# Performance work log

Measured on AMD Instinct MI355X. Metric: run time of the kernel, lower is better.

The kernel has to match this reference:

```python
import jax, jax.numpy as jnp
import numpy as np

B, T, D, H = 4, 2048, 512, 8
DK = D // H


def setup_inputs() -> dict:
    key0 = jax.random.key(0)
    ks = jax.random.split(key0, 16)
    s = 1.0 / np.sqrt(D)
    inp = {
        "query": jax.random.normal(ks[0], (B, T, D), jnp.float32),
        "key": jax.random.normal(ks[1], (B, T, D), jnp.float32),
        "value": jax.random.normal(ks[2], (B, T, D), jnp.float32),
        "mask": jnp.ones((B, 1, T), jnp.int32),
        "pos_emb": jax.random.normal(ks[3], (1, T, D), jnp.float32),
        "Wq": jax.random.normal(ks[4], (D, D), jnp.float32) * s,
        "bq": jnp.zeros((D,), jnp.float32),
        "Wk": jax.random.normal(ks[5], (D, D), jnp.float32) * s,
        "bk": jnp.zeros((D,), jnp.float32),
        "Wv": jax.random.normal(ks[6], (D, D), jnp.float32) * s,
        "bv": jnp.zeros((D,), jnp.float32),
        "Wo": jax.random.normal(ks[7], (D, D), jnp.float32) * s,
        "bo": jnp.zeros((D,), jnp.float32),
        "Wp": jax.random.normal(ks[8], (D, D), jnp.float32) * s,  # linear_pos, no bias
        "pos_bias_u": jax.random.normal(ks[9], (H, DK), jnp.float32) * 0.05,
        "pos_bias_v": jax.random.normal(ks[10], (H, DK), jnp.float32) * 0.05,
    }
    return inp


def reference(query, key, value, mask, pos_emb, Wq, bq, Wk, bk, Wv, bv, Wo, bo, Wp, pos_bias_u, pos_bias_v):
    b, t1, d = query.shape
    h, dk = pos_bias_u.shape
    # projections -> (b, t, h, dk)
    q = (query @ Wq.T + bq).reshape(b, t1, h, dk)
    k = (key @ Wk.T + bk).reshape(b, -1, h, dk)
    v = (value @ Wv.T + bv).reshape(b, -1, h, dk)
    # positional projection (n_batch_pos == 1): (t2, h, dk)
    p = (pos_emb @ Wp.T).reshape(pos_emb.shape[0], -1, h, dk)[0]
    # content score (a+c) and position score (b+d); NOTE: this repo's forward
    # does not apply rel_shift -- matrix_bd is used directly.
    matrix_ac = jnp.einsum("bthd,bshd->bhts", q + pos_bias_u, k)
    matrix_bd = jnp.einsum("bthd,shd->bhts", q + pos_bias_v, p)
    scores = (matrix_ac + matrix_bd) / np.sqrt(dk)
    # mask: (b, 1, t2) -> (b, 1, 1, t2); masked where mask == 0
    m = (mask[:, None, :, :] == 0)
    scores = jnp.where(m, -jnp.inf, scores)
    attn = jax.nn.softmax(scores, axis=-1)
    attn = jnp.where(m, 0.0, attn)
    x = jnp.einsum("bhts,bshd->bthd", attn, v).reshape(b, t1, h * dk)
    return x @ Wo.T + bo
```

## Files before the change

### kernel.cpp

```cpp
#include <hip/hip_runtime.h>

typedef __bf16 bf16;
typedef __attribute__((ext_vector_type(8))) __bf16 bf16x8;
typedef __attribute__((ext_vector_type(4))) __bf16 bf16x4;
typedef __attribute__((ext_vector_type(4))) float f32x4;

#define NB 4
#define NT 2048
#define ND 512
#define NH 8
#define NDK 64
#define GAMMA 0.1803368801111204f

#define OFF_XQ 0ull
#define OFF_XK 4194304ull
#define OFF_XV 8388608ull
#define OFF_XP 12582912ull
#define OFF_WQ 13631488ull
#define OFF_WK 13893632ull
#define OFF_WV 14155776ull
#define OFF_WP 14417920ull
#define OFF_WO 14680064ull
#define OFF_QU 14942208ull
#define OFF_QV 19136512ull
#define OFF_KB 23330816ull
#define OFF_VT 27525120ull
#define OFF_PB 31719424ull
#define OFF_OA OFF_XQ

__global__ __launch_bounds__(256) void convert_bf16(
    const float* __restrict__ q, const float* __restrict__ k,
    const float* __restrict__ v, const float* __restrict__ p,
    const float* __restrict__ wq, const float* __restrict__ wk,
    const float* __restrict__ wv, const float* __restrict__ wp,
    const float* __restrict__ wo, bf16* __restrict__ dst) {
  int bid = blockIdx.x;
  const float* src;
  size_t doff;
  if (bid < 2048) { src = q; doff = OFF_XQ; }
  else if (bid < 4096) { src = k; doff = OFF_XK; bid -= 2048; }
  else if (bid < 6144) { src = v; doff = OFF_XV; bid -= 4096; }
  else if (bid < 6656) { src = p; doff = OFF_XP; bid -= 6144; }
  else if (bid < 6784) { src = wq; doff = OFF_WQ; bid -= 6656; }
  else if (bid < 6912) { src = wk; doff = OFF_WK; bid -= 6784; }
  else if (bid < 7040) { src = wv; doff = OFF_WV; bid -= 6912; }
  else if (bid < 7168) { src = wp; doff = OFF_WP; bid -= 7040; }
  else { src = wo; doff = OFF_WO; bid -= 7168; }
  size_t base = (size_t)bid * 2048 + threadIdx.x * 8;
  float4 x0 = *(const float4*)(src + base);
  float4 x1 = *(const float4*)(src + base + 4);
  bf16x8 o;
  o[0] = (bf16)x0.x; o[1] = (bf16)x0.y; o[2] = (bf16)x0.z; o[3] = (bf16)x0.w;
  o[4] = (bf16)x1.x; o[5] = (bf16)x1.y; o[6] = (bf16)x1.z; o[7] = (bf16)x1.w;
  *(bf16x8*)(dst + doff + base) = o;
}

__device__ __forceinline__ void flush_tile(const bf16* LT, bf16* dst, int bm,
                                           int bn, int tid, bool isP) {
#pragma unroll
  for (int i = 0; i < 8; i++) {
    int chunk = tid + i * 256;
    int mm = chunk >> 4, c8 = (chunk & 15) * 8;
    bf16x8 vv = *(const bf16x8*)&LT[mm * 144 + c8];
    int n = bn + c8, h = n >> 6, d = n & 63;
    int gm = bm + mm;
    size_t gidx;
    if (isP)
      gidx = ((size_t)h * NT + gm) * NDK + d;
    else
      gidx = ((size_t)((gm >> 11) * NH + h) * NT + (gm & 2047)) * NDK + d;
    *(bf16x8*)(dst + gidx) = vv;
  }
}

__global__ __launch_bounds__(256) void proj_fused(
    const bf16* __restrict__ Xq, const bf16* __restrict__ Xk,
    const bf16* __restrict__ Xv, const bf16* __restrict__ Xp,
    const bf16* __restrict__ wq, const bf16* __restrict__ wk,
    const bf16* __restrict__ wv, const bf16* __restrict__ wp,
    const float* __restrict__ bq, const float* __restrict__ bk,
    const float* __restrict__ bv, const float* __restrict__ pu,
    const float* __restrict__ pv, bf16* __restrict__ Qu, bf16* __restrict__ Qv,
    bf16* __restrict__ Kb, bf16* __restrict__ Vt, bf16* __restrict__ Pb) {
  __shared__ bf16 smem[2][128][72];

  const int bid = blockIdx.x;
  const int mode = (bid >= 768) ? 3 : (bid >> 8);
  const int idx = (mode == 3) ? bid - 768 : (bid & 255);
  const int bm = (idx >> 2) * 128, bn = (idx & 3) * 128;

  const bf16* X;
  const bf16* W;
  if (mode == 0) { X = Xq; W = wq; }
  else if (mode == 1) { X = Xk; W = wk; }
  else if (mode == 2) { X = Xv; W = wv; }
  else { X = Xp; W = wp; }

  const int tid = threadIdx.x;
  const int l = tid & 63, w = tid >> 6;
  const int q = l >> 4, ln = l & 15;
  const int wm = (w >> 1) * 64, wn = (w & 1) * 64;

  f32x4 acc[4][4];
#pragma unroll
  for (int i = 0; i < 4; i++)
#pragma unroll
    for (int j = 0; j < 4; j++) acc[i][j] = (f32x4){0.f, 0.f, 0.f, 0.f};

  const int srow = tid >> 3, scol = (tid & 7) * 8;
  const size_t abase = (size_t)(bm + srow) * 512 + scol;
  const size_t bbase = (size_t)(bn + srow) * 512 + scol;

  bf16x8 ar[4], br[4];
#pragma unroll
  for (int i = 0; i < 4; i++) {
    ar[i] = *(const bf16x8*)(X + abase + (size_t)i * 32 * 512);
    br[i] = *(const bf16x8*)(W + bbase + (size_t)i * 32 * 512);
  }

  for (int k0 = 0; k0 < 512; k0 += 64) {
    __syncthreads();
#pragma unroll
    for (int i = 0; i < 4; i++) {
      *(bf16x8*)&smem[0][srow + i * 32][scol] = ar[i];
      *(bf16x8*)&smem[1][srow + i * 32][scol] = br[i];
    }
    if (k0 + 64 < 512) {
#pragma unroll
      for (int i = 0; i < 4; i++) {
        ar[i] = *(const bf16x8*)(X + abase + k0 + 64 + (size_t)i * 32 * 512);
        br[i] = *(const bf16x8*)(W + bbase + k0 + 64 + (size_t)i * 32 * 512);
      }
    }
    __syncthreads();
#pragma unroll
    for (int kc = 0; kc < 2; kc++) {
      bf16x8 af[4], bfr[4];
#pragma unroll
      for (int rt = 0; rt < 4; rt++)
        af[rt] = *(const bf16x8*)&smem[0][wm + rt * 16 + ln][kc * 32 + q * 8];
#pragma unroll
      for (int ct = 0; ct < 4; ct++)
        bfr[ct] = *(const bf16x8*)&smem[1][wn + ct * 16 + ln][kc * 32 + q * 8];
#pragma unroll
      for (int rt = 0; rt < 4; rt++)
#pragma unroll
        for (int ct = 0; ct < 4; ct++)
          acc[rt][ct] = __builtin_amdgcn_mfma_f32_16x16x32_bf16(
              af[rt], bfr[ct], acc[rt][ct], 0, 0, 0);
    }
  }

  bf16* LT = &smem[0][0][0];

  if (mode == 2) {
    __syncthreads();
#pragma unroll
    for (int ct = 0; ct < 4; ct++) {
      const int n = bn + wn + ct * 16 + ln;
      const float bvn = bv[n];
#pragma unroll
      for (int rt = 0; rt < 4; rt++) {
        bf16x4 t4;
#pragma unroll
        for (int r = 0; r < 4; r++) t4[r] = (bf16)(acc[rt][ct][r] + bvn);
        *(bf16x4*)&LT[(wn + ct * 16 + ln) * 144 + wm + rt * 16 + q * 4] = t4;
      }
    }
    __syncthreads();
    const int b = bm >> 11, tb = bm & 2047;
#pragma unroll
    for (int i = 0; i < 8; i++) {
      int chunk = tid + i * 256;
      int nn = chunk >> 4, m8 = (chunk & 15) * 8;
      int n = bn + nn, h = n >> 6, d = n & 63;
      size_t gidx = (((size_t)(b * NH + h)) * NDK + d) * NT + tb + m8;
      *(bf16x8*)(Vt + gidx) = *(const bf16x8*)&LT[nn * 144 + m8];
    }
    return;
  }

  if (mode == 0) {
    float addu[4], addv[4];
#pragma unroll
    for (int ct = 0; ct < 4; ct++) {
      int n = bn + wn + ct * 16 + ln;
      float bb = bq[n];
      addu[ct] = bb + pu[n];
      addv[ct] = bb + pv[n];
    }
    __syncthreads();
#pragma unroll
    for (int rt = 0; rt < 4; rt++)
#pragma unroll
      for (int ct = 0; ct < 4; ct++)
#pragma unroll
        for (int r = 0; r < 4; r++)
          LT[(wm + rt * 16 + q * 4 + r) * 144 + wn + ct * 16 + ln] =
              (bf16)((acc[rt][ct][r] + addu[ct]) * GAMMA);
    __syncthreads();
    flush_tile(LT, Qu, bm, bn, tid, false);
    __syncthreads();
#pragma unroll
    for (int rt = 0; rt < 4; rt++)
#pragma unroll
      for (int ct = 0; ct < 4; ct++)
#pragma unroll
        for (int r = 0; r < 4; r++)
          LT[(wm + rt * 16 + q * 4 + r) * 144 + wn + ct * 16 + ln] =
              (bf16)((acc[rt][ct][r] + addv[ct]) * GAMMA);
    __syncthreads();
    flush_tile(LT, Qv, bm, bn, tid, false);
    return;
  }

  {
    float bb[4];
#pragma unroll
    for (int ct = 0; ct < 4; ct++) {
      int n = bn + wn + ct * 16 + ln;
      bb[ct] = (mode == 1) ? bk[n] : 0.f;
    }
    __syncthreads();
#pragma unroll
    for (int rt = 0; rt < 4; rt++)
#pragma unroll
      for (int ct = 0; ct < 4; ct++)
#pragma unroll
        for (int r = 0; r < 4; r++)
          LT[(wm + rt * 16 + q * 4 + r) * 144 + wn + ct * 16 + ln] =
              (bf16)(acc[rt][ct][r] + bb[ct]);
    __syncthreads();
    flush_tile(LT, (mode == 1) ? Kb : Pb, bm, bn, tid, mode == 3);
  }
}

__global__ __launch_bounds__(256) void flash(
    const bf16* __restrict__ Qu, const bf16* __restrict__ Qv,
    const bf16* __restrict__ Kb, const bf16* __restrict__ Pb,
    const bf16* __restrict__ Vt, const int* __restrict__ mask,
    bf16* __restrict__ Oa) {
  __shared__ bf16 sK[64][136];
  __shared__ bf16 sVt[64][72];
  __shared__ bf16 sPT[4][16][40];
  __shared__ float sbias[64];

  const int tid = threadIdx.x;
  const int l = tid & 63, w = tid >> 6;
  const int q = l >> 4, ln = l & 15;
  const int t0 = blockIdx.x * 64;
  const int bh = blockIdx.y;
  const int b = bh >> 3;

  const size_t qrow = (((size_t)bh) * NT + t0 + w * 16 + ln) * NDK;
  bf16x8 qf[4];
  qf[0] = *(const bf16x8*)(Qu + qrow + q * 8);
  qf[1] = *(const bf16x8*)(Qu + qrow + 32 + q * 8);
  qf[2] = *(const bf16x8*)(Qv + qrow + q * 8);
  qf[3] = *(const bf16x8*)(Qv + qrow + 32 + q * 8);

  int okacc = 1;
  for (int i = tid; i < NT; i += 256) okacc &= (mask[b * NT + i] != 0);
  const int allones = __syncthreads_and(okacc);

  float lsum = 0.f;
  f32x4 O[4];
#pragma unroll
  for (int dt = 0; dt < 4; dt++) O[dt] = (f32x4){0.f, 0.f, 0.f, 0.f};

  const bf16* Krow = Kb + ((size_t)bh) * NT * NDK;
  const bf16* Prow = Pb + ((size_t)(bh & 7)) * NT * NDK;
  const bf16* Vrow = Vt + ((size_t)bh) * NDK * NT;

  const int krow = tid >> 4, kcc = tid & 15;
  const int vrow = tid >> 3, vcol = (tid & 7) * 8;
  const bf16* kpsrc = (kcc < 8) ? (Krow + kcc * 8) : (Prow + (kcc - 8) * 8);

  bf16x8 rk[4], rv[2];
#pragma unroll
  for (int i = 0; i < 4; i++)
    rk[i] = *(const bf16x8*)(kpsrc + (size_t)(krow + i * 16) * NDK);
#pragma unroll
  for (int i = 0; i < 2; i++)
    rv[i] = *(const bf16x8*)(Vrow + (size_t)(vrow + i * 32) * NT + vcol);

  for (int s0 = 0; s0 < NT; s0 += 64) {
    __syncthreads();
#pragma unroll
    for (int i = 0; i < 4; i++) *(bf16x8*)&sK[krow + i * 16][kcc * 8] = rk[i];
#pragma unroll
    for (int i = 0; i < 2; i++) *(bf16x8*)&sVt[vrow + i * 32][vcol] = rv[i];
    if (s0 + 64 < NT) {
#pragma unroll
      for (int i = 0; i < 4; i++)
        rk[i] =
            *(const bf16x8*)(kpsrc + (size_t)(s0 + 64 + krow + i * 16) * NDK);
#pragma unroll
      for (int i = 0; i < 2; i++)
        rv[i] = *(const bf16x8*)(Vrow + (size_t)(vrow + i * 32) * NT + s0 + 64 +
                                 vcol);
    }
    if (!allones && tid < 64)
      sbias[tid] = mask[b * NT + s0 + tid] ? 0.f : -1e30f;
    __syncthreads();

    f32x4 ST[4];
#pragma unroll
    for (int ct = 0; ct < 4; ct++) {
      ST[ct] = (f32x4){0.f, 0.f, 0.f, 0.f};
#pragma unroll
      for (int kc = 0; kc < 4; kc++) {
        bf16x8 kf = *(const bf16x8*)&sK[ct * 16 + ln][kc * 32 + q * 8];
        ST[ct] = __builtin_amdgcn_mfma_f32_16x16x32_bf16(kf, qf[kc], ST[ct], 0,
                                                         0, 0);
      }
    }
    if (!allones) {
#pragma unroll
      for (int ct = 0; ct < 4; ct++) {
        float4 bb = *(const float4*)&sbias[ct * 16 + q * 4];
        ST[ct][0] += bb.x;
        ST[ct][1] += bb.y;
        ST[ct][2] += bb.z;
        ST[ct][3] += bb.w;
      }
    }
#pragma unroll
    for (int c = 0; c < 2; c++) {
#pragma unroll
      for (int cc = 0; cc < 2; cc++) {
        const int ct = c * 2 + cc;
        unsigned u0 = __builtin_bit_cast(unsigned,
                                         __builtin_amdgcn_exp2f(ST[ct][0]));
        unsigned u1 = __builtin_bit_cast(unsigned,
                                         __builtin_amdgcn_exp2f(ST[ct][1]));
        unsigned u2 = __builtin_bit_cast(unsigned,
                                         __builtin_amdgcn_exp2f(ST[ct][2]));
        unsigned u3 = __builtin_bit_cast(unsigned,
                                         __builtin_amdgcn_exp2f(ST[ct][3]));
        lsum += __builtin_bit_cast(float, u0 & 0xffff0000u) +
                __builtin_bit_cast(float, u1 & 0xffff0000u) +
                __builtin_bit_cast(float, u2 & 0xffff0000u) +
                __builtin_bit_cast(float, u3 & 0xffff0000u);
        uint2 pk;
        pk.x = (u0 >> 16) | (u1 & 0xffff0000u);
        pk.y = (u2 >> 16) | (u3 & 0xffff0000u);
        *(uint2*)&sPT[w][ln][cc * 16 + q * 4] = pk;
      }
      bf16x8 paf = *(const bf16x8*)&sPT[w][ln][q * 8];
#pragma unroll
      for (int dt = 0; dt < 4; dt++) {
        bf16x8 vb = *(const bf16x8*)&sVt[dt * 16 + ln][c * 32 + q * 8];
        O[dt] =
            __builtin_amdgcn_mfma_f32_16x16x32_bf16(paf, vb, O[dt], 0, 0, 0);
      }
    }
  }

  float s = lsum;
  s += __shfl_xor(s, 16);
  s += __shfl_xor(s, 32);
#pragma unroll
  for (int r = 0; r < 4; r++) {
    float dr = __shfl(s, q * 4 + r);
    float inv = (dr > 0.f) ? 1.f / dr : 0.f;
    int t = t0 + w * 16 + q * 4 + r;
    size_t base = (((size_t)b * NT + t) * NH + (bh & 7)) * NDK;
#pragma unroll
    for (int dt = 0; dt < 4; dt++)
      Oa[base + dt * 16 + ln] = (bf16)(O[dt][r] * inv);
  }
}

__global__ __launch_bounds__(256) void out_gemm(const bf16* __restrict__ A,
                                                const bf16* __restrict__ W,
                                                const float* __restrict__ bias,
                                                float* __restrict__ out) {
  __shared__ bf16 sA[128][72];
  __shared__ bf16 sB[64][72];

  const int tid = threadIdx.x;
  const int l = tid & 63, w = tid >> 6;
  const int q = l >> 4, ln = l & 15;
  const int wm = (w >> 1) * 64, wn = (w & 1) * 32;
  const int bm = blockIdx.x * 128, bn = blockIdx.y * 64;

  f32x4 acc[4][2];
#pragma unroll
  for (int i = 0; i < 4; i++)
#pragma unroll
    for (int j = 0; j < 2; j++) acc[i][j] = (f32x4){0.f, 0.f, 0.f, 0.f};

  const int srow = tid >> 3, scol = (tid & 7) * 8;
  const size_t abase = (size_t)(bm + srow) * 512 + scol;
  const size_t bbase = (size_t)(bn + srow) * 512 + scol;

  bf16x8 ar[4], br[2];
#pragma unroll
  for (int i = 0; i < 4; i++)
    ar[i] = *(const bf16x8*)(A + abase + (size_t)i * 32 * 512);
#pragma unroll
  for (int i = 0; i < 2; i++)
    br[i] = *(const bf16x8*)(W + bbase + (size_t)i * 32 * 512);

  for (int k0 = 0; k0 < 512; k0 += 64) {
    __syncthreads();
#pragma unroll
    for (int i = 0; i < 4; i++) *(bf16x8*)&sA[srow + i * 32][scol] = ar[i];
#pragma unroll
    for (int i = 0; i < 2; i++) *(bf16x8*)&sB[srow + i * 32][scol] = br[i];
    if (k0 + 64 < 512) {
#pragma unroll
      for (int i = 0; i < 4; i++)
        ar[i] = *(const bf16x8*)(A + abase + k0 + 64 + (size_t)i * 32 * 512);
#pragma unroll
      for (int i = 0; i < 2; i++)
        br[i] = *(const bf16x8*)(W + bbase + k0 + 64 + (size_t)i * 32 * 512);
    }
    __syncthreads();
#pragma unroll
    for (int kc = 0; kc < 2; kc++) {
      bf16x8 af[4], bfr[2];
#pragma unroll
      for (int rt = 0; rt < 4; rt++)
        af[rt] = *(const bf16x8*)&sA[wm + rt * 16 + ln][kc * 32 + q * 8];
#pragma unroll
      for (int ct = 0; ct < 2; ct++)
        bfr[ct] = *(const bf16x8*)&sB[wn + ct * 16 + ln][kc * 32 + q * 8];
#pragma unroll
      for (int rt = 0; rt < 4; rt++)
#pragma unroll
        for (int ct = 0; ct < 2; ct++)
          acc[rt][ct] = __builtin_amdgcn_mfma_f32_16x16x32_bf16(
              af[rt], bfr[ct], acc[rt][ct], 0, 0, 0);
    }
  }

#pragma unroll
  for (int rt = 0; rt < 4; rt++)
#pragma unroll
    for (int ct = 0; ct < 2; ct++) {
      const int n = bn + wn + ct * 16 + ln;
      const float bias_n = bias[n];
#pragma unroll
      for (int r = 0; r < 4; r++) {
        const int m = bm + wm + rt * 16 + q * 4 + r;
        out[(size_t)m * 512 + n] = acc[rt][ct][r] + bias_n;
      }
    }
}

extern "C" void kernel_launch(void* const* d_in, const int* in_sizes, int n_in,
                              void* d_out, int out_size, void* d_ws,
                              size_t ws_size, hipStream_t stream) {
  const float* query = (const float*)d_in[0];
  const float* key = (const float*)d_in[1];
  const float* value = (const float*)d_in[2];
  const int* mask = (const int*)d_in[3];
  const float* pos = (const float*)d_in[4];
  const float* Wq = (const float*)d_in[5];
  const float* bq = (const float*)d_in[6];
  const float* Wk = (const float*)d_in[7];
  const float* bk = (const float*)d_in[8];
  const float* Wv = (const float*)d_in[9];
  const float* bv = (const float*)d_in[10];
  const float* Wo = (const float*)d_in[11];
  const float* bo = (const float*)d_in[12];
  const float* Wp = (const float*)d_in[13];
  const float* pu = (const float*)d_in[14];
  const float* pv = (const float*)d_in[15];
  float* out = (float*)d_out;

  bf16* ws = (bf16*)d_ws;
  dim3 blk(256);
  convert_bf16<<<dim3(7296), blk, 0, stream>>>(query, key, value, pos, Wq, Wk,
                                               Wv, Wp, Wo, ws);
  proj_fused<<<dim3(832), blk, 0, stream>>>(
      ws + OFF_XQ, ws + OFF_XK, ws + OFF_XV, ws + OFF_XP, ws + OFF_WQ,
      ws + OFF_WK, ws + OFF_WV, ws + OFF_WP, bq, bk, bv, pu, pv, ws + OFF_QU,
      ws + OFF_QV, ws + OFF_KB, ws + OFF_VT, ws + OFF_PB);
  flash<<<dim3(32, 32), blk, 0, stream>>>(ws + OFF_QU, ws + OFF_QV,
                                          ws + OFF_KB, ws + OFF_PB,
                                          ws + OFF_VT, mask, ws + OFF_OA);
  out_gemm<<<dim3(64, 8), blk, 0, stream>>>(ws + OFF_OA, ws + OFF_WO, bo, out);
}
```

Baseline: 248.0 us.

## Enlarge flash blocks to 1024 threads and vectorize projection epilogue stores

The flash kernel now runs 16 waves per block covering 256 query rows, so each K/P/V tile staged in shared memory is reused by four times as many query rows, and each thread loads one K row chunk and at most one V chunk per step. The projection GEMM swaps the MFMA operands for non-V modes so each lane holds four consecutive columns. That lets the epilogue write bf16x4 vectors with float4 bias loads, and the padded LDS strides change to reduce bank conflicts. In exchange, the large flash blocks lower per-block scheduling flexibility, give only 256 blocks, and put register pressure under 1024-thread launch bounds.

```diff
diff --git a/kernel.cpp b/kernel.cpp
--- a/kernel.cpp
+++ b/kernel.cpp
@@ -11,6 +11,7 @@
 #define NH 8
 #define NDK 64
 #define GAMMA 0.1803368801111204f
+#define LTS 152
 
 #define OFF_XQ 0ull
 #define OFF_XK 4194304ull
@@ -61,7 +62,7 @@
   for (int i = 0; i < 8; i++) {
     int chunk = tid + i * 256;
     int mm = chunk >> 4, c8 = (chunk & 15) * 8;
-    bf16x8 vv = *(const bf16x8*)&LT[mm * 144 + c8];
+    bf16x8 vv = *(const bf16x8*)&LT[mm * LTS + c8];
     int n = bn + c8, h = n >> 6, d = n & 63;
     int gm = bm + mm;
     size_t gidx;
@@ -82,7 +83,7 @@
     const float* __restrict__ bv, const float* __restrict__ pu,
     const float* __restrict__ pv, bf16* __restrict__ Qu, bf16* __restrict__ Qv,
     bf16* __restrict__ Kb, bf16* __restrict__ Vt, bf16* __restrict__ Pb) {
-  __shared__ bf16 smem[2][128][72];
+  __shared__ bf16 smem[2][128][76];
 
   const int bid = blockIdx.x;
   const int mode = (bid >= 768) ? 3 : (bid >> 8);
@@ -142,12 +143,21 @@
 #pragma unroll
       for (int ct = 0; ct < 4; ct++)
         bfr[ct] = *(const bf16x8*)&smem[1][wn + ct * 16 + ln][kc * 32 + q * 8];
-#pragma unroll
-      for (int rt = 0; rt < 4; rt++)
-#pragma unroll
-        for (int ct = 0; ct < 4; ct++)
-          acc[rt][ct] = __builtin_amdgcn_mfma_f32_16x16x32_bf16(
-              af[rt], bfr[ct], acc[rt][ct], 0, 0, 0);
+      if (mode == 2) {
+#pragma unroll
+        for (int rt = 0; rt < 4; rt++)
+#pragma unroll
+          for (int ct = 0; ct < 4; ct++)
+            acc[rt][ct] = __builtin_amdgcn_mfma_f32_16x16x32_bf16(
+                af[rt], bfr[ct], acc[rt][ct], 0, 0, 0);
+      } else {
+#pragma unroll
+        for (int rt = 0; rt < 4; rt++)
+#pragma unroll
+          for (int ct = 0; ct < 4; ct++)
+            acc[rt][ct] = __builtin_amdgcn_mfma_f32_16x16x32_bf16(
+                bfr[ct], af[rt], acc[rt][ct], 0, 0, 0);
+      }
     }
   }
 
@@ -164,7 +174,7 @@
         bf16x4 t4;
 #pragma unroll
         for (int r = 0; r < 4; r++) t4[r] = (bf16)(acc[rt][ct][r] + bvn);
-        *(bf16x4*)&LT[(wn + ct * 16 + ln) * 144 + wm + rt * 16 + q * 4] = t4;
+        *(bf16x4*)&LT[(wn + ct * 16 + ln) * LTS + wm + rt * 16 + q * 4] = t4;
       }
     }
     __syncthreads();
@@ -175,84 +185,98 @@
       int nn = chunk >> 4, m8 = (chunk & 15) * 8;
       int n = bn + nn, h = n >> 6, d = n & 63;
       size_t gidx = (((size_t)(b * NH + h)) * NDK + d) * NT + tb + m8;
-      *(bf16x8*)(Vt + gidx) = *(const bf16x8*)&LT[nn * 144 + m8];
+      *(bf16x8*)(Vt + gidx) = *(const bf16x8*)&LT[nn * LTS + m8];
     }
     return;
   }
 
+  const int mloc = wm + ln;
+  const int nloc = wn + q * 4;
+
   if (mode == 0) {
-    float addu[4], addv[4];
+    float4 addu4[4], addv4[4];
 #pragma unroll
     for (int ct = 0; ct < 4; ct++) {
-      int n = bn + wn + ct * 16 + ln;
-      float bb = bq[n];
-      addu[ct] = bb + pu[n];
-      addv[ct] = bb + pv[n];
+      int n0 = bn + nloc + ct * 16;
+      float4 bb = *(const float4*)(bq + n0);
+      float4 uu = *(const float4*)(pu + n0);
+      float4 vv = *(const float4*)(pv + n0);
+      addu4[ct] = make_float4(bb.x + uu.x, bb.y + uu.y, bb.z + uu.z, bb.w + uu.w);
+      addv4[ct] = make_float4(bb.x + vv.x, bb.y + vv.y, bb.z + vv.z, bb.w + vv.w);
     }
     __syncthreads();
 #pragma unroll
     for (int rt = 0; rt < 4; rt++)
 #pragma unroll
-      for (int ct = 0; ct < 4; ct++)
+      for (int ct = 0; ct < 4; ct++) {
+        const float* au = &addu4[ct].x;
+        bf16x4 t4;
 #pragma unroll
         for (int r = 0; r < 4; r++)
-          LT[(wm + rt * 16 + q * 4 + r) * 144 + wn + ct * 16 + ln] =
-              (bf16)((acc[rt][ct][r] + addu[ct]) * GAMMA);
+          t4[r] = (bf16)((acc[rt][ct][r] + au[r]) * GAMMA);
+        *(bf16x4*)&LT[(mloc + rt * 16) * LTS + nloc + ct * 16] = t4;
+      }
     __syncthreads();
     flush_tile(LT, Qu, bm, bn, tid, false);
     __syncthreads();
 #pragma unroll
     for (int rt = 0; rt < 4; rt++)
 #pragma unroll
-      for (int ct = 0; ct < 4; ct++)
+      for (int ct = 0; ct < 4; ct++) {
+        const float* av = &addv4[ct].x;
+        bf16x4 t4;
 #pragma unroll
         for (int r = 0; r < 4; r++)
-          LT[(wm + rt * 16 + q * 4 + r) * 144 + wn + ct * 16 + ln] =
-              (bf16)((acc[rt][ct][r] + addv[ct]) * GAMMA);
+          t4[r] = (bf16)((acc[rt][ct][r] + av[r]) * GAMMA);
+        *(bf16x4*)&LT[(mloc + rt * 16) * LTS + nloc + ct * 16] = t4;
+      }
     __syncthreads();
     flush_tile(LT, Qv, bm, bn, tid, false);
     return;
   }
 
   {
-    float bb[4];
+    float4 bb4[4];
 #pragma unroll
     for (int ct = 0; ct < 4; ct++) {
-      int n = bn + wn + ct * 16 + ln;
-      bb[ct] = (mode == 1) ? bk[n] : 0.f;
+      int n0 = bn + nloc + ct * 16;
+      bb4[ct] = (mode == 1) ? *(const float4*)(bk + n0)
+                            : make_float4(0.f, 0.f, 0.f, 0.f);
     }
     __syncthreads();
 #pragma unroll
     for (int rt = 0; rt < 4; rt++)
 #pragma unroll
-      for (int ct = 0; ct < 4; ct++)
-#pragma unroll
-        for (int r = 0; r < 4; r++)
-          LT[(wm + rt * 16 + q * 4 + r) * 144 + wn + ct * 16 + ln] =
-              (bf16)(acc[rt][ct][r] + bb[ct]);
+      for (int ct = 0; ct < 4; ct++) {
+        const float* bbp = &bb4[ct].x;
+        bf16x4 t4;
+#pragma unroll
+        for (int r = 0; r < 4; r++) t4[r] = (bf16)(acc[rt][ct][r] + bbp[r]);
+        *(bf16x4*)&LT[(mloc + rt * 16) * LTS + nloc + ct * 16] = t4;
+      }
     __syncthreads();
     flush_tile(LT, (mode == 1) ? Kb : Pb, bm, bn, tid, mode == 3);
   }
 }
 
-__global__ __launch_bounds__(256) void flash(
+__global__ __launch_bounds__(1024) void flash(
     const bf16* __restrict__ Qu, const bf16* __restrict__ Qv,
     const bf16* __restrict__ Kb, const bf16* __restrict__ Pb,
     const bf16* __restrict__ Vt, const int* __restrict__ mask,
     bf16* __restrict__ Oa) {
   __shared__ bf16 sK[64][136];
   __shared__ bf16 sVt[64][72];
-  __shared__ bf16 sPT[4][16][40];
+  __shared__ bf16 sPT[16][16][40];
   __shared__ float sbias[64];
 
   const int tid = threadIdx.x;
-  const int l = tid & 63, w = tid >> 6;
+  const int l = tid & 63, wv = tid >> 6;
   const int q = l >> 4, ln = l & 15;
-  const int t0 = blockIdx.x * 64;
-  const int bh = blockIdx.y;
+  const int bh = blockIdx.x;
+  const int t0 = blockIdx.y * 256;
   const int b = bh >> 3;
 
-  const size_t qrow = (((size_t)bh) * NT + t0 + w * 16 + ln) * NDK;
+  const size_t qrow = (((size_t)bh) * NT + t0 + wv * 16 + ln) * NDK;
   bf16x8 qf[4];
   qf[0] = *(const bf16x8*)(Qu + qrow + q * 8);
   qf[1] = *(const bf16x8*)(Qu + qrow + 32 + q * 8);
@@ -260,7 +284,7 @@
   qf[3] = *(const bf16x8*)(Qv + qrow + 32 + q * 8);
 
   int okacc = 1;
-  for (int i = tid; i < NT; i += 256) okacc &= (mask[b * NT + i] != 0);
+  for (int i = tid; i < NT; i += 1024) okacc &= (mask[b * NT + i] != 0);
   const int allones = __syncthreads_and(okacc);
 
   float lsum = 0.f;
@@ -273,32 +297,22 @@
   const bf16* Vrow = Vt + ((size_t)bh) * NDK * NT;
 
   const int krow = tid >> 4, kcc = tid & 15;
-  const int vrow = tid >> 3, vcol = (tid & 7) * 8;
+  const int vrow = (tid & 511) >> 3, vcol = (tid & 7) * 8;
+  const bool doV = (tid < 512);
   const bf16* kpsrc = (kcc < 8) ? (Krow + kcc * 8) : (Prow + (kcc - 8) * 8);
 
-  bf16x8 rk[4], rv[2];
-#pragma unroll
-  for (int i = 0; i < 4; i++)
-    rk[i] = *(const bf16x8*)(kpsrc + (size_t)(krow + i * 16) * NDK);
-#pragma unroll
-  for (int i = 0; i < 2; i++)
-    rv[i] = *(const bf16x8*)(Vrow + (size_t)(vrow + i * 32) * NT + vcol);
+  bf16x8 rk, rv;
+  rk = *(const bf16x8*)(kpsrc + (size_t)krow * NDK);
+  if (doV) rv = *(const bf16x8*)(Vrow + (size_t)vrow * NT + vcol);
 
   for (int s0 = 0; s0 < NT; s0 += 64) {
     __syncthreads();
-#pragma unroll
-    for (int i = 0; i < 4; i++) *(bf16x8*)&sK[krow + i * 16][kcc * 8] = rk[i];
-#pragma unroll
-    for (int i = 0; i < 2; i++) *(bf16x8*)&sVt[vrow + i * 32][vcol] = rv[i];
+    *(bf16x8*)&sK[krow][kcc * 8] = rk;
+    if (doV) *(bf16x8*)&sVt[vrow][vcol] = rv;
     if (s0 + 64 < NT) {
-#pragma unroll
-      for (int i = 0; i < 4; i++)
-        rk[i] =
-            *(const bf16x8*)(kpsrc + (size_t)(s0 + 64 + krow + i * 16) * NDK);
-#pragma unroll
-      for (int i = 0; i < 2; i++)
-        rv[i] = *(const bf16x8*)(Vrow + (size_t)(vrow + i * 32) * NT + s0 + 64 +
-                                 vcol);
+      rk = *(const bf16x8*)(kpsrc + (size_t)(s0 + 64 + krow) * NDK);
+      if (doV)
+        rv = *(const bf16x8*)(Vrow + (size_t)vrow * NT + s0 + 64 + vcol);
     }
     if (!allones && tid < 64)
       sbias[tid] = mask[b * NT + s0 + tid] ? 0.f : -1e30f;
@@ -330,14 +344,14 @@
 #pragma unroll
       for (int cc = 0; cc < 2; cc++) {
         const int ct = c * 2 + cc;
-        unsigned u0 = __builtin_bit_cast(unsigned,
-                                         __builtin_amdgcn_exp2f(ST[ct][0]));
-        unsigned u1 = __builtin_bit_cast(unsigned,
-                                         __builtin_amdgcn_exp2f(ST[ct][1]));
-        unsigned u2 = __builtin_bit_cast(unsigned,
-                                         __builtin_amdgcn_exp2f(ST[ct][2]));
-        unsigned u3 = __builtin_bit_cast(unsigned,
-                                         __builtin_amdgcn_exp2f(ST[ct][3]));
+        unsigned u0 =
+            __builtin_bit_cast(unsigned, __builtin_amdgcn_exp2f(ST[ct][0]));
+        unsigned u1 =
+            __builtin_bit_cast(unsigned, __builtin_amdgcn_exp2f(ST[ct][1]));
+        unsigned u2 =
+            __builtin_bit_cast(unsigned, __builtin_amdgcn_exp2f(ST[ct][2]));
+        unsigned u3 =
+            __builtin_bit_cast(unsigned, __builtin_amdgcn_exp2f(ST[ct][3]));
         lsum += __builtin_bit_cast(float, u0 & 0xffff0000u) +
                 __builtin_bit_cast(float, u1 & 0xffff0000u) +
                 __builtin_bit_cast(float, u2 & 0xffff0000u) +
@@ -345,9 +359,9 @@
         uint2 pk;
         pk.x = (u0 >> 16) | (u1 & 0xffff0000u);
         pk.y = (u2 >> 16) | (u3 & 0xffff0000u);
-        *(uint2*)&sPT[w][ln][cc * 16 + q * 4] = pk;
-      }
-      bf16x8 paf = *(const bf16x8*)&sPT[w][ln][q * 8];
+        *(uint2*)&sPT[wv][ln][cc * 16 + q * 4] = pk;
+      }
+      bf16x8 paf = *(const bf16x8*)&sPT[wv][ln][q * 8];
 #pragma unroll
       for (int dt = 0; dt < 4; dt++) {
         bf16x8 vb = *(const bf16x8*)&sVt[dt * 16 + ln][c * 32 + q * 8];
@@ -364,7 +378,7 @@
   for (int r = 0; r < 4; r++) {
     float dr = __shfl(s, q * 4 + r);
     float inv = (dr > 0.f) ? 1.f / dr : 0.f;
-    int t = t0 + w * 16 + q * 4 + r;
+    int t = t0 + wv * 16 + q * 4 + r;
     size_t base = (((size_t)b * NT + t) * NH + (bh & 7)) * NDK;
 #pragma unroll
     for (int dt = 0; dt < 4; dt++)
@@ -479,8 +493,8 @@
       ws + OFF_XQ, ws + OFF_XK, ws + OFF_XV, ws + OFF_XP, ws + OFF_WQ,
       ws + OFF_WK, ws + OFF_WV, ws + OFF_WP, bq, bk, bv, pu, pv, ws + OFF_QU,
       ws + OFF_QV, ws + OFF_KB, ws + OFF_VT, ws + OFF_PB);
-  flash<<<dim3(32, 32), blk, 0, stream>>>(ws + OFF_QU, ws + OFF_QV,
-                                          ws + OFF_KB, ws + OFF_PB,
-                                          ws + OFF_VT, mask, ws + OFF_OA);
+  flash<<<dim3(32, 8), dim3(1024), 0, stream>>>(ws + OFF_QU, ws + OFF_QV,
+                                                ws + OFF_KB, ws + OFF_PB,
+                                                ws + OFF_VT, mask, ws + OFF_OA);
   out_gemm<<<dim3(64, 8), blk, 0, stream>>>(ws + OFF_OA, ws + OFF_WO, bo, out);
 }
```

Result: faster. 241.9 us (-2.4%).
